# Kernel tuning notes

Hardware: AMD Instinct MI355X
Metric: run time of the kernel (lower is better)

## Reference

```python
import jax, jax.numpy as jnp
import numpy as np

TAU = 0.1


def setup_inputs() -> dict:
    key = jax.random.key(0)
    k1, k2, k3 = jax.random.split(key, 3)
    B, C, H, W = 32, 1, 512, 512
    input1 = jax.random.normal(k1, (B, C, H, W), dtype=jnp.float32)
    input2 = jax.random.normal(k2, (B, C, H, W), dtype=jnp.float32)
    mask = jax.random.uniform(k3, (B, C, H, W), dtype=jnp.float32)
    return {"input1": input1, "input2": input2, "mask": mask}


def reference(input1, input2, mask):
    # logit=True: apply sigmoid first
    x1 = jax.nn.sigmoid(input1)
    x2 = jax.nn.sigmoid(input2)
    B = x1.shape[0]
    N = x1.shape[1] * x1.shape[2] * x1.shape[3]

    # positive similarity: masked MSE per sample over (C,H,W)
    sim_pos = jnp.exp(-jnp.mean((mask * (x1 - x2)) ** 2, axis=(1, 2, 3)) / TAU)

    # negative similarities: all-pairs MSE via GEMM expansion trick
    # mean((a-b)^2) = (|a|^2 + |b|^2 - 2 a.b) / N
    f1 = x1.reshape(B, N)
    f2 = x2.reshape(B, N)
    sq1 = jnp.sum(f1 * f1, axis=1)  # [B]
    sq2 = jnp.sum(f2 * f2, axis=1)  # [B]
    cross = f1 @ f2.T               # [B,B]
    d = (sq1[:, None] + sq2[None, :] - 2.0 * cross) / N
    sim = jnp.exp(-d / TAU)         # [B,B]
    # exclude b1 == b2 diagonal terms
    sim_neg = jnp.sum(sim, axis=1) - jnp.diagonal(sim)

    loss = -jnp.log(sim_pos / (sim_pos + sim_neg))
    return jnp.mean(loss)
```

## Files before the change

### kernel.cpp

```cpp
#include <hip/hip_runtime.h>
#include <hip/hip_bf16.h>

#define NF 262144
#define NROWS 32
#define BK 64
#define TPB 4
#define SLICE 1120
#define NSLICES 16

typedef __attribute__((ext_vector_type(8))) __bf16 bf16x8;
typedef __attribute__((ext_vector_type(16))) float f32x16;

__device__ __forceinline__ float sigmoid_fast(float x) {
    float e = __expf(-x);
    return __builtin_amdgcn_rcpf(1.0f + e);
}

__device__ __forceinline__ void gload16(const float* g, float* l) {
    __builtin_amdgcn_global_load_lds(
        (const __attribute__((address_space(1))) void*)g,
        (__attribute__((address_space(3))) void*)l, 16, 0, 0);
}

__global__ __launch_bounds__(256, 3) void cl_main(const float* __restrict__ in1,
                                                  const float* __restrict__ in2,
                                                  const float* __restrict__ msk,
                                                  float* __restrict__ ws) {
    __shared__ float smem[12288];

    const int tid  = threadIdx.x;
    const int w    = tid >> 6;
    const int lane = tid & 63;
    const int r    = lane & 31;
    const int g    = lane >> 5;
    const int jr   = lane >> 4;
    const int jc   = lane & 15;
    const int rsw  = r & 15;

    const float* arrs[3] = {in1, in2, msk};

    f32x16 acc;
    #pragma unroll
    for (int k = 0; k < 16; ++k) acc[k] = 0.0f;
    float pos = 0.0f, q1 = 0.0f, q2 = 0.0f;

    const int colbase = blockIdx.x * (TPB * BK);

    auto stage = [&](int p, int t) {
        const int coloff = colbase + t * BK;
        #pragma unroll
        for (int k = 0; k < 6; ++k) {
            const int n   = w * 6 + k;
            const int a   = n >> 3;
            const int q   = n & 7;
            const int row = q * 4 + jr;
            gload16(arrs[a] + (size_t)row * NF + coloff + ((jc ^ (row & 15)) << 2),
                    smem + p * 6144 + a * 2048 + q * 256);
        }
    };

    auto compute = [&](int p) {
        const int c1 = w * 4 + g * 2;
        const float* base = smem + p * 6144 + r * 64;
        float4 A0 = *(const float4*)(base +        ((c1       ^ rsw) << 2));
        float4 A1 = *(const float4*)(base +        (((c1 + 1) ^ rsw) << 2));
        float4 B0 = *(const float4*)(base + 2048 + ((c1       ^ rsw) << 2));
        float4 B1 = *(const float4*)(base + 2048 + (((c1 + 1) ^ rsw) << 2));
        float4 M0 = *(const float4*)(base + 4096 + ((c1       ^ rsw) << 2));
        float4 M1 = *(const float4*)(base + 4096 + (((c1 + 1) ^ rsw) << 2));

        float xa[8], xb[8], xm[8];
        *(float4*)&xa[0] = A0; *(float4*)&xa[4] = A1;
        *(float4*)&xb[0] = B0; *(float4*)&xb[4] = B1;
        *(float4*)&xm[0] = M0; *(float4*)&xm[4] = M1;

        bf16x8 fa, fb;
        #pragma unroll
        for (int e = 0; e < 8; ++e) {
            float sa = sigmoid_fast(xa[e]);
            float sb = sigmoid_fast(xb[e]);
            float d  = xm[e] * (sa - sb);
            pos = fmaf(d, d, pos);
            q1  = fmaf(sa, sa, q1);
            q2  = fmaf(sb, sb, q2);
            fa[e] = (__bf16)sa;
            fb[e] = (__bf16)sb;
        }
        acc = __builtin_amdgcn_mfma_f32_32x32x16_bf16(fa, fb, acc, 0, 0, 0);
    };

    stage(0, 0);
    __syncthreads();
    #pragma unroll
    for (int t = 0; t < TPB - 1; ++t) {
        stage((t + 1) & 1, t + 1);
        compute(t & 1);
        __syncthreads();
    }
    compute((TPB - 1) & 1);

    float* s_c = smem;
    float* s_v = smem + 4096;
    const int col = lane & 31;
    const int rhi = (lane >> 5) * 4;
    #pragma unroll
    for (int reg = 0; reg < 16; ++reg) {
        const int row = (reg & 3) + 8 * (reg >> 2) + rhi;
        s_c[w * 1024 + row * 32 + col] = acc[reg];
    }
    pos += __shfl_down(pos, 32);
    q1  += __shfl_down(q1, 32);
    q2  += __shfl_down(q2, 32);
    if (lane < 32) {
        s_v[w * 96 + r]      = pos;
        s_v[w * 96 + 32 + r] = q1;
        s_v[w * 96 + 64 + r] = q2;
    }
    __syncthreads();

    float* slice = ws + (size_t)(blockIdx.x & (NSLICES - 1)) * SLICE;
    for (int idx = tid; idx < 1024; idx += 256) {
        float s = s_c[idx] + s_c[1024 + idx] + s_c[2048 + idx] + s_c[3072 + idx];
        atomicAdd(&slice[idx], s);
    }
    if (tid < 96) {
        float s = s_v[tid] + s_v[96 + tid] + s_v[192 + tid] + s_v[288 + tid];
        atomicAdd(&slice[1024 + tid], s);
    }
}

__global__ __launch_bounds__(1024) void cl_final(const float* __restrict__ ws,
                                                 float* __restrict__ out) {
    __shared__ float s_loss[32];
    const int tid = threadIdx.x;
    const int i = tid >> 5, j = tid & 31;
    const float invN = 1.0f / (float)NF;

    float c = 0.0f, p = 0.0f, s1 = 0.0f, s2 = 0.0f;
    #pragma unroll
    for (int k = 0; k < NSLICES; ++k) {
        const float* sl = ws + (size_t)k * SLICE;
        c  += sl[i * 32 + j];
        p  += sl[1024 + i];
        s1 += sl[1056 + i];
        s2 += sl[1088 + j];
    }

    float d = (s1 + s2 - 2.0f * c) * invN;
    float sim = (i == j) ? 0.0f : expf(-d * 10.0f);
    #pragma unroll
    for (int off = 16; off; off >>= 1) sim += __shfl_xor(sim, off);

    if (j == 0) {
        float sp = expf(-p * invN * 10.0f);
        s_loss[i] = -logf(sp / (sp + sim));
    }
    __syncthreads();
    if (tid == 0) {
        float t = 0.0f;
        #pragma unroll
        for (int k = 0; k < 32; ++k) t += s_loss[k];
        out[0] = t * (1.0f / 32.0f);
    }
}

extern "C" void kernel_launch(void* const* d_in, const int* in_sizes, int n_in,
                              void* d_out, int out_size, void* d_ws, size_t ws_size,
                              hipStream_t stream) {
    const float* in1 = (const float*)d_in[0];
    const float* in2 = (const float*)d_in[1];
    const float* msk = (const float*)d_in[2];
    float* out = (float*)d_out;
    float* ws  = (float*)d_ws;

    hipMemsetAsync(ws, 0, NSLICES * SLICE * sizeof(float), stream);
    cl_main<<<1024, 256, 0, stream>>>(in1, in2, msk, ws);
    cl_final<<<1, 1024, 0, stream>>>(ws, out);
}
```

Baseline: 44.99 us.

## Replace atomic slice accumulation with per-block partials and a reduce kernel

```diff
diff --git a/kernel.cpp b/kernel.cpp
--- a/kernel.cpp
+++ b/kernel.cpp
@@ -5,8 +5,9 @@
 #define NROWS 32
 #define BK 64
 #define TPB 4
-#define SLICE 1120
-#define NSLICES 16
+#define NBLK 1024
+#define PSTRIDE 1152
+#define NKG 16
 
 typedef __attribute__((ext_vector_type(8))) __bf16 bf16x8;
 typedef __attribute__((ext_vector_type(16))) float f32x16;
@@ -118,18 +119,29 @@
     }
     __syncthreads();
 
-    float* slice = ws + (size_t)(blockIdx.x & (NSLICES - 1)) * SLICE;
+    float* P = ws + (size_t)blockIdx.x * PSTRIDE;
     for (int idx = tid; idx < 1024; idx += 256) {
-        float s = s_c[idx] + s_c[1024 + idx] + s_c[2048 + idx] + s_c[3072 + idx];
-        atomicAdd(&slice[idx], s);
+        P[idx] = s_c[idx] + s_c[1024 + idx] + s_c[2048 + idx] + s_c[3072 + idx];
     }
     if (tid < 96) {
-        float s = s_v[tid] + s_v[96 + tid] + s_v[192 + tid] + s_v[288 + tid];
-        atomicAdd(&slice[1024 + tid], s);
+        P[1024 + tid] = s_v[tid] + s_v[96 + tid] + s_v[192 + tid] + s_v[288 + tid];
     }
 }
 
-__global__ __launch_bounds__(1024) void cl_final(const float* __restrict__ ws,
+__global__ __launch_bounds__(256) void cl_reduce(const float* __restrict__ ws,
+                                                 float* __restrict__ out2) {
+    const int kg   = blockIdx.x / 5;
+    const int sg   = blockIdx.x % 5;
+    const int slot = sg * 256 + threadIdx.x;
+    if (slot >= 1120) return;
+    const float* base = ws + (size_t)kg * 64 * PSTRIDE + slot;
+    float s = 0.0f;
+    #pragma unroll 8
+    for (int k = 0; k < 64; ++k) s += base[(size_t)k * PSTRIDE];
+    out2[kg * PSTRIDE + slot] = s;
+}
+
+__global__ __launch_bounds__(1024) void cl_final(const float* __restrict__ ws2,
                                                  float* __restrict__ out) {
     __shared__ float s_loss[32];
     const int tid = threadIdx.x;
@@ -138,8 +150,8 @@
 
     float c = 0.0f, p = 0.0f, s1 = 0.0f, s2 = 0.0f;
     #pragma unroll
-    for (int k = 0; k < NSLICES; ++k) {
-        const float* sl = ws + (size_t)k * SLICE;
+    for (int k = 0; k < NKG; ++k) {
+        const float* sl = ws2 + (size_t)k * PSTRIDE;
         c  += sl[i * 32 + j];
         p  += sl[1024 + i];
         s1 += sl[1056 + i];
@@ -172,8 +184,9 @@
     const float* msk = (const float*)d_in[2];
     float* out = (float*)d_out;
     float* ws  = (float*)d_ws;
+    float* ws2 = ws + (size_t)NBLK * PSTRIDE;
 
-    hipMemsetAsync(ws, 0, NSLICES * SLICE * sizeof(float), stream);
-    cl_main<<<1024, 256, 0, stream>>>(in1, in2, msk, ws);
-    cl_final<<<1, 1024, 0, stream>>>(ws, out);
+    cl_main  <<<NBLK, 256, 0, stream>>>(in1, in2, msk, ws);
+    cl_reduce<<<80,   256, 0, stream>>>(ws, ws2);
+    cl_final <<<1,   1024, 0, stream>>>(ws2, out);
 }
```

Measured after the change: 44.94 us. No clear change (-0.1%).
